# Optimization experiments

Measured on AMD Instinct MI355X. Metric: run time of the kernel, lower is better.

Reference implementation:

```python
import jax, jax.numpy as jnp
import numpy as np

N_NODES = 100000
N_EDGES = 1600000
D_IN, D_HID, D_OUT = 64, 64, 2


def setup_inputs() -> dict:
    key = jax.random.key(0)
    k1, k2, k3, k4 = jax.random.split(key, 4)
    x = jax.random.normal(k1, (N_NODES, D_IN), dtype=jnp.float32)
    edge_index = jax.random.randint(k2, (2, N_EDGES), 0, N_NODES, dtype=jnp.int64)
    W1 = jax.random.normal(k3, (D_IN, D_HID), dtype=jnp.float32) * (1.0 / np.sqrt(D_IN))
    b1 = jnp.zeros((D_HID,), dtype=jnp.float32)
    W2 = jax.random.normal(k4, (D_HID, D_OUT), dtype=jnp.float32) * (1.0 / np.sqrt(D_HID))
    b2 = jnp.zeros((D_OUT,), dtype=jnp.float32)
    return {"x": x, "edge_index": edge_index, "W1": W1, "b1": b1, "W2": W2, "b2": b2}


def _gcn_norm(edge_index, num_nodes):
    # PyG GCNConv default: add self-loops, symmetric normalization D^-1/2 (A+I) D^-1/2
    loops = jnp.arange(num_nodes, dtype=edge_index.dtype)
    row = jnp.concatenate([edge_index[0], loops])  # source
    col = jnp.concatenate([edge_index[1], loops])  # destination
    deg = jax.ops.segment_sum(jnp.ones_like(col, dtype=jnp.float32), col, num_segments=num_nodes)
    dinv = jnp.where(deg > 0, jax.lax.rsqrt(deg), 0.0)
    norm = dinv[row] * dinv[col]  # [E + N]
    return row, col, norm


def _gcn_conv(x, W, b, row, col, norm, num_nodes):
    h = x @ W                              # [N, D_out] small GEMM first (PyG order)
    msg = h[row] * norm[:, None]           # gather + scale  [E+N, D_out]
    out = jax.ops.segment_sum(msg, col, num_segments=num_nodes)  # scatter-add
    return out + b


def reference(x, edge_index, W1, b1, W2, b2):
    n = x.shape[0]
    row, col, norm = _gcn_norm(edge_index, n)
    h = jax.nn.relu(_gcn_conv(x, W1, b1, row, col, norm, n))
    return _gcn_conv(h, W2, b2, row, col, norm, n)
```

## Files before the change

kernel.cpp:

```cpp
#include <hip/hip_runtime.h>


#define D_IN 64
#define NBBITS 10
#define NBK_PAD 128
#define PCH 8192
#define BCAP 16384
#define BCAPE 24576

__device__ __forceinline__ float b2f(unsigned short u) {
    unsigned v = ((unsigned)u) << 16;
    float f;
    __builtin_memcpy(&f, &v, 4);
    return f;
}
__device__ __forceinline__ unsigned short f2b(float f) {
    unsigned u;
    __builtin_memcpy(&u, &f, 4);
    u += 0x7FFFu + ((u >> 16) & 1u);
    return (unsigned short)(u >> 16);
}

__device__ __forceinline__ int edge_val(const int* __restrict__ p, int f64, long pos) {
    return f64 ? p[2 * pos] : p[pos];
}

__device__ __forceinline__ void acc8(float* a, uint4 rv, float wgt) {
    a[0] = fmaf(wgt, b2f((unsigned short)(rv.x & 0xFFFFu)), a[0]);
    a[1] = fmaf(wgt, b2f((unsigned short)(rv.x >> 16)), a[1]);
    a[2] = fmaf(wgt, b2f((unsigned short)(rv.y & 0xFFFFu)), a[2]);
    a[3] = fmaf(wgt, b2f((unsigned short)(rv.y >> 16)), a[3]);
    a[4] = fmaf(wgt, b2f((unsigned short)(rv.z & 0xFFFFu)), a[4]);
    a[5] = fmaf(wgt, b2f((unsigned short)(rv.z >> 16)), a[5]);
    a[6] = fmaf(wgt, b2f((unsigned short)(rv.w & 0xFFFFu)), a[6]);
    a[7] = fmaf(wgt, b2f((unsigned short)(rv.w >> 16)), a[7]);
}

__global__ __launch_bounds__(256, 4) void k_part_gemm(
        const int* __restrict__ ep, int* __restrict__ bptr,
        unsigned* __restrict__ ebuf,
        const float* __restrict__ x, const float* __restrict__ W,
        unsigned short* __restrict__ H, int E, int N, int nPart) {
    __shared__ __align__(16) char smraw[34816];
    int tid = threadIdx.x;

    if (blockIdx.x < nPart) {
        int* hist  = (int*)smraw;
        int* lofs  = hist + NBK_PAD;
        int* gbase = lofs + NBK_PAD;
        int* fsh   = gbase + NBK_PAD;
        unsigned* stage = (unsigned*)(fsh + 4);

        if (tid < NBK_PAD) hist[tid] = 0;
        if (tid < 64) {
            int bad = 0;
            for (int i = tid; i < 1024; i += 64)
                if (ep[2 * i + 1] != 0) bad = 1;
            unsigned long long m = __ballot(bad);
            if (tid == 0) fsh[0] = (m == 0ull) ? 1 : 0;
        }
        __syncthreads();
        int f = fsh[0];
        long base = (long)blockIdx.x * PCH;
        for (int i = tid; i < PCH; i += 256) {
            long e = base + i;
            if (e < E) {
                int c = edge_val(ep, f, E + e);
                atomicAdd(&hist[c >> NBBITS], 1);
            }
        }
        __syncthreads();
        if (tid < NBK_PAD) lofs[tid] = hist[tid];
        __syncthreads();
        for (int off = 1; off < NBK_PAD; off <<= 1) {
            int t = (tid < NBK_PAD && tid >= off) ? lofs[tid - off] : 0;
            __syncthreads();
            if (tid < NBK_PAD) lofs[tid] += t;
            __syncthreads();
        }
        if (tid < NBK_PAD) { lofs[tid] -= hist[tid]; hist[tid] = 0; }
        __syncthreads();
        for (int i = tid; i < PCH; i += 256) {
            long e = base + i;
            if (e < E) {
                int c = edge_val(ep, f, E + e);
                int r = edge_val(ep, f, e);
                int b = c >> NBBITS;
                int pos = lofs[b] + atomicAdd(&hist[b], 1);
                stage[pos] = (unsigned)r | ((unsigned)(c & ((1 << NBBITS) - 1)) << 17);
            }
        }
        __syncthreads();
        if (tid < NBK_PAD && hist[tid]) gbase[tid] = atomicAdd(&bptr[tid], hist[tid]);
        __syncthreads();
        int wid = tid >> 6, lane = tid & 63;
        for (int b = wid; b < NBK_PAD; b += 4) {
            int c = hist[b];
            if (c == 0) continue;
            int lo = lofs[b], go = gbase[b];
            unsigned* dst = ebuf + (size_t)b * BCAPE + go;
            for (int j = lane; j < c; j += 64) dst[j] = stage[lo + j];
        }
    } else {
        float* Ws = (float*)smraw;
        float* Xs = (float*)(smraw + 16384);
        int lane = tid & 63;
        int wv = tid >> 6;
        for (int i = tid; i < 64 * 64; i += 256) Ws[i] = W[i];

        int bid = blockIdx.x - nPart;
        int ngb = gridDim.x - nPart;
        int ntiles = (N + 31) >> 5;
        for (int tile = bid; tile < ntiles; tile += ngb) {
            int rr = tid >> 4, c4 = tid & 15;
            int g0 = (tile << 5) + rr;
            int g1 = g0 + 16;
            float4 v0 = make_float4(0.f, 0.f, 0.f, 0.f);
            float4 v1 = make_float4(0.f, 0.f, 0.f, 0.f);
            if (g0 < N) v0 = *(const float4*)(x + (size_t)g0 * 64 + c4 * 4);
            if (g1 < N) v1 = *(const float4*)(x + (size_t)g1 * 64 + c4 * 4);
            __syncthreads();
            *(float4*)(&Xs[rr * 68 + c4 * 4]) = v0;
            *(float4*)(&Xs[(rr + 16) * 68 + c4 * 4]) = v1;
            __syncthreads();
            float acc[8];
            #pragma unroll
            for (int r = 0; r < 8; ++r) acc[r] = 0.f;
            int rbase = wv * 8;
            #pragma unroll 4
            for (int k4 = 0; k4 < 16; ++k4) {
                float w0 = Ws[(4 * k4 + 0) * 64 + lane];
                float w1 = Ws[(4 * k4 + 1) * 64 + lane];
                float w2 = Ws[(4 * k4 + 2) * 64 + lane];
                float w3 = Ws[(4 * k4 + 3) * 64 + lane];
                #pragma unroll
                for (int r = 0; r < 8; ++r) {
                    float4 xq = *(const float4*)(&Xs[(rbase + r) * 68 + k4 * 4]);
                    acc[r] = fmaf(xq.x, w0, acc[r]);
                    acc[r] = fmaf(xq.y, w1, acc[r]);
                    acc[r] = fmaf(xq.z, w2, acc[r]);
                    acc[r] = fmaf(xq.w, w3, acc[r]);
                }
            }
            int row0 = (tile << 5) + rbase;
            #pragma unroll
            for (int r = 0; r < 8; ++r) {
                int row = row0 + r;
                if (row < N) H[(size_t)row * 64 + lane] = f2b(acc[r]);
            }
        }
    }
}

__global__ __launch_bounds__(1024) void k_bucket(const unsigned* __restrict__ ebuf,
                                                 const int* __restrict__ bptr,
                                                 int* __restrict__ offs,
                                                 float* __restrict__ dinv,
                                                 int* __restrict__ srcA, int N, int E) {
    __shared__ int hist[1024], escan[1024], wsum[16];
    __shared__ int bco[NBK_PAD];
    __shared__ int stage[BCAP];
    int tid = threadIdx.x, b = blockIdx.x;
    int lane = tid & 63, wid = tid >> 6;
    hist[tid] = 0;
    if (tid < NBK_PAD) {
        int c = bptr[tid];
        int s = c;
        #pragma unroll
        for (int off = 1; off < 64; off <<= 1) {
            int t = __shfl(s, lane - off);
            if (lane >= off) s += t;
        }
        if (lane == 63) wsum[wid] = s;
        bco[tid] = s - c;
    }
    if (tid == 0 && b == 0) offs[N] = E;
    __syncthreads();
    if (tid >= 64 && tid < NBK_PAD) bco[tid] += wsum[0];
    __syncthreads();

    int rbase = b * BCAPE;
    int lo = bco[b];
    int m = bptr[b];
    for (int i = tid; i < m; i += 1024) {
        unsigned w = ebuf[rbase + i];
        atomicAdd(&hist[w >> 17], 1);
    }
    __syncthreads();
    int v = hist[tid];
    int s = v;
    #pragma unroll
    for (int off = 1; off < 64; off <<= 1) {
        int t = __shfl(s, lane - off);
        if (lane >= off) s += t;
    }
    if (lane == 63) wsum[wid] = s;
    __syncthreads();
    if (tid < 16) {
        int xv = wsum[tid];
        int ss = xv;
        #pragma unroll
        for (int off = 1; off < 16; off <<= 1) {
            int t = __shfl(ss, lane - off);
            if (lane >= off) ss += t;
        }
        wsum[tid] = ss - xv;
    }
    __syncthreads();
    int excl = s - v + wsum[wid];
    escan[tid] = excl;
    int g = (b << NBBITS) + tid;
    if (g < N) {
        offs[g] = lo + excl;
        dinv[g] = rsqrtf((float)(v + 1));
    }
    __syncthreads();
    for (int i = tid; i < m; i += 1024) {
        unsigned w = ebuf[rbase + i];
        int lc = w >> 17;
        int src = (int)(w & 0x1FFFFu);
        int sl = escan[lc] + atomicSub(&hist[lc], 1) - 1;
        if (sl < BCAP) stage[sl] = src;
        else srcA[lo + sl] = src;
    }
    __syncthreads();
    int mm = min(m, BCAP);
    for (int i = tid; i < mm; i += 1024) srcA[lo + i] = stage[i];
}

__global__ void k_agg1(const unsigned short* __restrict__ H1,
                       const int* __restrict__ srcA,
                       const float* __restrict__ dinv, const int* __restrict__ offs,
                       const float* __restrict__ b1, const float* __restrict__ W2,
                       float* __restrict__ Z, int N) {
    int wid = (blockIdx.x * blockDim.x + threadIdx.x) >> 6;
    int lane = threadIdx.x & 63;
    int g = lane >> 3, s = lane & 7;
    int n = wid * 8 + g;
    bool nvalid = (n < N);
    int nn = nvalid ? n : 0;
    float dn = dinv[nn];
    int base = offs[nn];
    int cnt = nvalid ? (offs[nn + 1] - base) : 0;
    int cm = cnt;
    #pragma unroll
    for (int off = 8; off <= 32; off <<= 1) cm = max(cm, __shfl_xor(cm, off));
    float a[8];
    #pragma unroll
    for (int k = 0; k < 8; ++k) a[k] = 0.f;
    const uint4* H4 = (const uint4*)H1;
    int gb = g << 3;
    for (int j0 = 0; j0 < cm; j0 += 8) {
        int sv = 0; float wl = 0.f;
        if (j0 + s < cnt) { sv = srcA[base + j0 + s]; wl = dinv[sv]; }
        int   s0 = __shfl(sv, gb + 0), s1 = __shfl(sv, gb + 1);
        int   s2 = __shfl(sv, gb + 2), s3 = __shfl(sv, gb + 3);
        int   s4 = __shfl(sv, gb + 4), s5 = __shfl(sv, gb + 5);
        int   s6 = __shfl(sv, gb + 6), s7 = __shfl(sv, gb + 7);
        float w0 = __shfl(wl, gb + 0), w1 = __shfl(wl, gb + 1);
        float w2 = __shfl(wl, gb + 2), w3 = __shfl(wl, gb + 3);
        float w4 = __shfl(wl, gb + 4), w5 = __shfl(wl, gb + 5);
        float w6 = __shfl(wl, gb + 6), w7 = __shfl(wl, gb + 7);
        uint4 r0 = H4[(size_t)s0 * 8 + s];
        uint4 r1 = H4[(size_t)s1 * 8 + s];
        uint4 r2 = H4[(size_t)s2 * 8 + s];
        uint4 r3 = H4[(size_t)s3 * 8 + s];
        uint4 r4 = H4[(size_t)s4 * 8 + s];
        uint4 r5 = H4[(size_t)s5 * 8 + s];
        uint4 r6 = H4[(size_t)s6 * 8 + s];
        uint4 r7 = H4[(size_t)s7 * 8 + s];
        acc8(a, r0, w0); acc8(a, r1, w1); acc8(a, r2, w2); acc8(a, r3, w3);
        acc8(a, r4, w4); acc8(a, r5, w5); acc8(a, r6, w6); acc8(a, r7, w7);
    }
    uint4 rs = H4[(size_t)nn * 8 + s];
    acc8(a, rs, dn);
    float4 b1a = *(const float4*)(b1 + s * 8);
    float4 b1b = *(const float4*)(b1 + s * 8 + 4);
    float h0 = fmaxf(dn * a[0] + b1a.x, 0.f);
    float h1 = fmaxf(dn * a[1] + b1a.y, 0.f);
    float h2 = fmaxf(dn * a[2] + b1a.z, 0.f);
    float h3 = fmaxf(dn * a[3] + b1a.w, 0.f);
    float h4 = fmaxf(dn * a[4] + b1b.x, 0.f);
    float h5 = fmaxf(dn * a[5] + b1b.y, 0.f);
    float h6 = fmaxf(dn * a[6] + b1b.z, 0.f);
    float h7 = fmaxf(dn * a[7] + b1b.w, 0.f);
    const float4* w2p = (const float4*)(W2 + s * 16);
    float4 q0 = w2p[0], q1 = w2p[1], q2 = w2p[2], q3 = w2p[3];
    float p0 = h0 * q0.x + h1 * q0.z + h2 * q1.x + h3 * q1.z
             + h4 * q2.x + h5 * q2.z + h6 * q3.x + h7 * q3.z;
    float p1 = h0 * q0.y + h1 * q0.w + h2 * q1.y + h3 * q1.w
             + h4 * q2.y + h5 * q2.w + h6 * q3.y + h7 * q3.w;
    #pragma unroll
    for (int off = 1; off < 8; off <<= 1) {
        p0 += __shfl_xor(p0, off);
        p1 += __shfl_xor(p1, off);
    }
    if (s == 0 && nvalid) { Z[n * 2 + 0] = p0; Z[n * 2 + 1] = p1; }
}

__global__ void k_agg2(const float* __restrict__ Z, const int* __restrict__ srcA,
                       const float* __restrict__ dinv, const int* __restrict__ offs,
                       const float* __restrict__ b2, float* __restrict__ out, int N) {
    int t = blockIdx.x * blockDim.x + threadIdx.x;
    int lane = threadIdx.x & 63;
    int n = (t >> 6) * 4 + (lane >> 4);
    int sl = lane & 15;
    if (n >= N) return;
    int base = offs[n];
    int cnt = offs[n + 1] - base;
    float a0 = 0.f, a1 = 0.f;
    const float2* Z2 = (const float2*)Z;
    for (int i = sl; i < cnt; i += 16) {
        int src = srcA[base + i];
        float w = dinv[src];
        float2 zv = Z2[src];
        a0 += w * zv.x;
        a1 += w * zv.y;
    }
    #pragma unroll
    for (int off = 8; off > 0; off >>= 1) {
        a0 += __shfl_xor(a0, off);
        a1 += __shfl_xor(a1, off);
    }
    if (sl == 0) {
        float dn = dinv[n];
        float2 zs = Z2[n];
        out[n * 2 + 0] = dn * (a0 + dn * zs.x) + b2[0];
        out[n * 2 + 1] = dn * (a1 + dn * zs.y) + b2[1];
    }
}

extern "C" void kernel_launch(void* const* d_in, const int* in_sizes, int n_in,
                              void* d_out, int out_size, void* d_ws, size_t ws_size,
                              hipStream_t stream) {
    const float* x  = (const float*)d_in[0];
    const int*   ep = (const int*)d_in[1];
    const float* W1 = (const float*)d_in[2];
    const float* b1 = (const float*)d_in[3];
    const float* W2 = (const float*)d_in[4];
    const float* b2 = (const float*)d_in[5];
    float* out = (float*)d_out;

    const int N = in_sizes[0] / D_IN;
    const int E = in_sizes[1] / 2;

    char* ws = (char*)d_ws;
    size_t o = 0;
    auto alloc = [&](size_t bytes) {
        size_t r = o;
        o = (o + bytes + 255) & ~(size_t)255;
        return r;
    };
    int*            bptr  = (int*)           (ws + alloc(NBK_PAD * 4));
    float*          dinv  = (float*)         (ws + alloc((size_t)N * 4));
    int*            offs  = (int*)           (ws + alloc((size_t)(N + 1) * 4));
    unsigned*       ebuf  = (unsigned*)      (ws + alloc((size_t)NBK_PAD * BCAPE * 4));
    int*            srcA  = (int*)           (ws + alloc((size_t)E * 4));
    unsigned short* H1    = (unsigned short*)(ws + alloc((size_t)N * 64 * 2));
    float*          Z     = (float*)         (ws + alloc((size_t)N * 2 * 4));

    const int nbk = (N + (1 << NBBITS) - 1) >> NBBITS;
    const int nPart = (E + PCH - 1) / PCH;
    const int nGemm = 1024;

    (void)hipMemsetAsync(bptr, 0, NBK_PAD * sizeof(int), stream);
    k_part_gemm<<<nPart + nGemm, 256, 0, stream>>>(ep, bptr, ebuf, x, W1, H1, E, N, nPart);
    k_bucket<<<nbk, 1024, 0, stream>>>(ebuf, bptr, offs, dinv, srcA, N, E);
    int nwav = (N + 7) / 8;
    k_agg1<<<(nwav + 3) / 4, 256, 0, stream>>>(H1, srcA, dinv, offs, b1, W2, Z, N);
    k_agg2<<<(N + 15) / 16, 256, 0, stream>>>(Z, srcA, dinv, offs, b2, out, N);
}
```

Baseline: 106.1 us.

## Widen partition/GEMM blocks to 1024 threads with vectorized edge loads and wave-scan

The fused partition+GEMM kernel now runs 1024-thread blocks. Each partition thread loads its 8 edges with uint4 vector loads, keeping them in registers for both the histogram and scatter passes instead of reloading. The 128-bucket prefix scan uses wave shuffles instead of a barrier-heavy shared-memory loop. GEMM tiles grow to 128 rows and the total grid shrinks to about 512 blocks, which reduces block count but increases shared-memory use and register pressure per block.

```diff
diff --git a/kernel.cpp b/kernel.cpp
--- a/kernel.cpp
+++ b/kernel.cpp
@@ -36,13 +36,14 @@
     a[7] = fmaf(wgt, b2f((unsigned short)(rv.w >> 16)), a[7]);
 }
 
-__global__ __launch_bounds__(256, 4) void k_part_gemm(
+__global__ __launch_bounds__(1024, 8) void k_part_gemm(
         const int* __restrict__ ep, int* __restrict__ bptr,
         unsigned* __restrict__ ebuf,
         const float* __restrict__ x, const float* __restrict__ W,
         unsigned short* __restrict__ H, int E, int N, int nPart) {
-    __shared__ __align__(16) char smraw[34816];
+    __shared__ __align__(16) char smraw[51200];
     int tid = threadIdx.x;
+    int lane = tid & 63;
 
     if (blockIdx.x < nPart) {
         int* hist  = (int*)smraw;
@@ -62,39 +63,92 @@
         __syncthreads();
         int f = fsh[0];
         long base = (long)blockIdx.x * PCH;
-        for (int i = tid; i < PCH; i += 256) {
-            long e = base + i;
-            if (e < E) {
-                int c = edge_val(ep, f, E + e);
-                atomicAdd(&hist[c >> NBBITS], 1);
-            }
-        }
-        __syncthreads();
-        if (tid < NBK_PAD) lofs[tid] = hist[tid];
-        __syncthreads();
-        for (int off = 1; off < NBK_PAD; off <<= 1) {
-            int t = (tid < NBK_PAD && tid >= off) ? lofs[tid - off] : 0;
-            __syncthreads();
-            if (tid < NBK_PAD) lofs[tid] += t;
-            __syncthreads();
-        }
-        if (tid < NBK_PAD) { lofs[tid] -= hist[tid]; hist[tid] = 0; }
-        __syncthreads();
-        for (int i = tid; i < PCH; i += 256) {
-            long e = base + i;
-            if (e < E) {
-                int c = edge_val(ep, f, E + e);
-                int r = edge_val(ep, f, e);
+        long rem64 = (long)E - base;
+        int nE = rem64 > PCH ? PCH : (int)rem64;
+        int j0 = tid * 8;
+        int nv = nE - j0;
+        nv = nv < 0 ? 0 : (nv > 8 ? 8 : nv);
+        unsigned cc[8], rr2[8];
+        #pragma unroll
+        for (int k = 0; k < 8; ++k) { cc[k] = 0; rr2[k] = 0; }
+        bool fullv = (nv == 8);
+        const uint4* p4 = (const uint4*)ep;
+        if (f) {
+            if (fullv && ((E & 1) == 0)) {
+                size_t cb = ((size_t)E + (size_t)base + j0) >> 1;
+                uint4 a0 = p4[cb + 0], a1 = p4[cb + 1];
+                uint4 a2 = p4[cb + 2], a3 = p4[cb + 3];
+                cc[0] = a0.x; cc[1] = a0.z; cc[2] = a1.x; cc[3] = a1.z;
+                cc[4] = a2.x; cc[5] = a2.z; cc[6] = a3.x; cc[7] = a3.z;
+            } else {
+                for (int k = 0; k < 8; ++k)
+                    if (k < nv) cc[k] = (unsigned)ep[2 * ((size_t)E + base + j0 + k)];
+            }
+        } else {
+            if (fullv && ((E & 3) == 0)) {
+                size_t cb = ((size_t)E + (size_t)base + j0) >> 2;
+                uint4 a0 = p4[cb + 0], a1 = p4[cb + 1];
+                cc[0] = a0.x; cc[1] = a0.y; cc[2] = a0.z; cc[3] = a0.w;
+                cc[4] = a1.x; cc[5] = a1.y; cc[6] = a1.z; cc[7] = a1.w;
+            } else {
+                for (int k = 0; k < 8; ++k)
+                    if (k < nv) cc[k] = (unsigned)ep[(size_t)E + base + j0 + k];
+            }
+        }
+        #pragma unroll
+        for (int k = 0; k < 8; ++k)
+            if (k < nv) atomicAdd(&hist[cc[k] >> NBBITS], 1);
+        if (f) {
+            if (fullv && ((E & 1) == 0)) {
+                size_t rb = ((size_t)base + j0) >> 1;
+                uint4 b0 = p4[rb + 0], b1 = p4[rb + 1];
+                uint4 b2 = p4[rb + 2], b3 = p4[rb + 3];
+                rr2[0] = b0.x; rr2[1] = b0.z; rr2[2] = b1.x; rr2[3] = b1.z;
+                rr2[4] = b2.x; rr2[5] = b2.z; rr2[6] = b3.x; rr2[7] = b3.z;
+            } else {
+                for (int k = 0; k < 8; ++k)
+                    if (k < nv) rr2[k] = (unsigned)ep[2 * ((size_t)base + j0 + k)];
+            }
+        } else {
+            if (fullv && ((E & 3) == 0)) {
+                size_t rb = ((size_t)base + j0) >> 2;
+                uint4 b0 = p4[rb + 0], b1 = p4[rb + 1];
+                rr2[0] = b0.x; rr2[1] = b0.y; rr2[2] = b0.z; rr2[3] = b0.w;
+                rr2[4] = b1.x; rr2[5] = b1.y; rr2[6] = b1.z; rr2[7] = b1.w;
+            } else {
+                for (int k = 0; k < 8; ++k)
+                    if (k < nv) rr2[k] = (unsigned)ep[(size_t)base + j0 + k];
+            }
+        }
+        __syncthreads();
+        if (tid < NBK_PAD) {
+            int c = hist[tid], s = c;
+            #pragma unroll
+            for (int off = 1; off < 64; off <<= 1) {
+                int t2 = __shfl(s, lane - off);
+                if (lane >= off) s += t2;
+            }
+            if (lane == 63) fsh[1 + (tid >> 6)] = s;
+            lofs[tid] = s - c;
+        }
+        __syncthreads();
+        if (tid >= 64 && tid < NBK_PAD) lofs[tid] += fsh[1];
+        if (tid < NBK_PAD) hist[tid] = 0;
+        __syncthreads();
+        #pragma unroll
+        for (int k = 0; k < 8; ++k) {
+            if (k < nv) {
+                unsigned c = cc[k];
                 int b = c >> NBBITS;
                 int pos = lofs[b] + atomicAdd(&hist[b], 1);
-                stage[pos] = (unsigned)r | ((unsigned)(c & ((1 << NBBITS) - 1)) << 17);
+                stage[pos] = rr2[k] | ((c & ((1u << NBBITS) - 1)) << 17);
             }
         }
         __syncthreads();
         if (tid < NBK_PAD && hist[tid]) gbase[tid] = atomicAdd(&bptr[tid], hist[tid]);
         __syncthreads();
-        int wid = tid >> 6, lane = tid & 63;
-        for (int b = wid; b < NBK_PAD; b += 4) {
+        int wv = tid >> 6;
+        for (int b = wv; b < NBK_PAD; b += 16) {
             int c = hist[b];
             if (c == 0) continue;
             int lo = lofs[b], go = gbase[b];
@@ -104,24 +158,23 @@
     } else {
         float* Ws = (float*)smraw;
         float* Xs = (float*)(smraw + 16384);
-        int lane = tid & 63;
         int wv = tid >> 6;
-        for (int i = tid; i < 64 * 64; i += 256) Ws[i] = W[i];
+        for (int i = tid; i < 64 * 64; i += 1024) Ws[i] = W[i];
 
         int bid = blockIdx.x - nPart;
         int ngb = gridDim.x - nPart;
-        int ntiles = (N + 31) >> 5;
+        int ntiles = (N + 127) >> 7;
         for (int tile = bid; tile < ntiles; tile += ngb) {
             int rr = tid >> 4, c4 = tid & 15;
-            int g0 = (tile << 5) + rr;
-            int g1 = g0 + 16;
+            int g0 = (tile << 7) + rr;
+            int g1 = g0 + 64;
             float4 v0 = make_float4(0.f, 0.f, 0.f, 0.f);
             float4 v1 = make_float4(0.f, 0.f, 0.f, 0.f);
             if (g0 < N) v0 = *(const float4*)(x + (size_t)g0 * 64 + c4 * 4);
             if (g1 < N) v1 = *(const float4*)(x + (size_t)g1 * 64 + c4 * 4);
             __syncthreads();
             *(float4*)(&Xs[rr * 68 + c4 * 4]) = v0;
-            *(float4*)(&Xs[(rr + 16) * 68 + c4 * 4]) = v1;
+            *(float4*)(&Xs[(rr + 64) * 68 + c4 * 4]) = v1;
             __syncthreads();
             float acc[8];
             #pragma unroll
@@ -142,7 +195,7 @@
                     acc[r] = fmaf(xq.w, w3, acc[r]);
                 }
             }
-            int row0 = (tile << 5) + rbase;
+            int row0 = (tile << 7) + rbase;
             #pragma unroll
             for (int r = 0; r < 8; ++r) {
                 int row = row0 + r;
@@ -361,10 +414,11 @@
 
     const int nbk = (N + (1 << NBBITS) - 1) >> NBBITS;
     const int nPart = (E + PCH - 1) / PCH;
-    const int nGemm = 1024;
+    int nGemm = 512 - nPart;
+    if (nGemm < 64) nGemm = 64;
 
     (void)hipMemsetAsync(bptr, 0, NBK_PAD * sizeof(int), stream);
-    k_part_gemm<<<nPart + nGemm, 256, 0, stream>>>(ep, bptr, ebuf, x, W1, H1, E, N, nPart);
+    k_part_gemm<<<nPart + nGemm, 1024, 0, stream>>>(ep, bptr, ebuf, x, W1, H1, E, N, nPart);
     k_bucket<<<nbk, 1024, 0, stream>>>(ebuf, bptr, offs, dinv, srcA, N, E);
     int nwav = (N + 7) / 8;
     k_agg1<<<(nwav + 3) / 4, 256, 0, stream>>>(H1, srcA, dinv, offs, b1, W2, Z, N);
```

Measured after the change: 104.5 us. About the same (-1.5%).
